# Optimization experiments

Hardware: AMD Instinct MI355X
Metric: run time of the kernel (lower is better)

## Reference

```python
import jax, jax.numpy as jnp
import numpy as np

THRESH = 1.0
SLOPE = 25.0  # fast_sigmoid surrogate slope
B, T, C_IN = 64, 512, 32
HID, TS, K = 128, 4, 3
C_OUT = HID * TS

@jax.custom_vjp
def spike_fn(x):
    # Heaviside forward, fast-sigmoid surrogate backward (matches snntorch surrogate.fast_sigmoid(slope=25))
    return (x > 0).astype(x.dtype)

def _spike_fwd(x):
    return spike_fn(x), x

def _spike_bwd(x, g):
    return (g / (SLOPE * jnp.abs(x) + 1.0) ** 2,)

spike_fn.defvjp(_spike_fwd, _spike_bwd)


def setup_inputs() -> dict:
    key = jax.random.key(0)
    ks = jax.random.split(key, 4)
    return {
        "x": jax.random.normal(ks[0], (B, T, C_IN), jnp.float32),
        "conv_w": jax.random.normal(ks[1], (C_OUT, C_IN, K), jnp.float32) / np.sqrt(C_IN * K).astype(np.float32),
        "conv_b": jax.random.normal(ks[2], (C_OUT,), jnp.float32) * 0.01,
        "bn_gamma": jnp.ones((C_OUT,), jnp.float32),
        "bn_beta": jnp.zeros((C_OUT,), jnp.float32),
        "bn_mean": jax.random.normal(ks[3], (C_OUT,), jnp.float32) * 0.1,
        "bn_var": jnp.ones((C_OUT,), jnp.float32),
        "lif_beta": jnp.full((HID,), 0.9, jnp.float32),
    }


def reference(x, conv_w, conv_b, bn_gamma, bn_beta, bn_mean, bn_var, lif_beta):
    # Conv1d(input -> hidden*Ts, k=3, pad=1): x (B,T,C) -> NCH layout
    h = jax.lax.conv_general_dilated(
        x.transpose(0, 2, 1), conv_w, (1,), [(K // 2, K // 2)],
        dimension_numbers=("NCH", "OIH", "NCH"))  # (B, C_OUT, T)
    h = h + conv_b[None, :, None]
    # BatchNorm1d in eval mode (running stats)
    scale = bn_gamma * jax.lax.rsqrt(bn_var + 1e-5)
    h = (h - bn_mean[None, :, None]) * scale[None, :, None] + bn_beta[None, :, None]
    # (B, C_OUT, T) -> (B, T, Ts, HID) -> (Ts*T, B, HID) time-major spike input
    h = h.transpose(0, 2, 1).reshape(B, T * TS, HID).transpose(1, 0, 2)

    beta = jnp.clip(lif_beta, 0.0, 1.0)

    def step(mem, h_t):
        # snntorch Leaky (reset_mechanism='subtract'): reset from previous mem, detached
        reset = jax.lax.stop_gradient((mem > THRESH).astype(mem.dtype))
        mem = beta * mem + h_t - reset * THRESH
        spk = spike_fn(mem - THRESH)
        return mem, (spk, mem)

    mem0 = jnp.zeros((B, HID), x.dtype)
    _, (spk_rec, mem_rec) = jax.lax.scan(step, mem0, h)
    return spk_rec, mem_rec  # each (Ts*T, B, HID)
```

## Files before the change

kernel.cpp:

```cpp
#include <hip/hip_runtime.h>

#define T_LEN 512
#define CIN   32
#define HIDN  128
#define TSUB  4
#define NB    64
#define TT    64
#define NT2   2048
#define COLS  8192

#define HT_IDX(s, col, t) ((((size_t)(s) * COLS + (size_t)(col)) * T_LEN) + (size_t)(t))

__global__ __launch_bounds__(256) void conv_bn_kernel(
    const float* __restrict__ x,
    const float* __restrict__ w,
    const float* __restrict__ cb,
    const float* __restrict__ gam,
    const float* __restrict__ bet,
    const float* __restrict__ mean,
    const float* __restrict__ var,
    float* __restrict__ hT)
{
    __shared__ float xs[66 * 36];
    __shared__ float ws[64 * 100];
    __shared__ float scs[64];
    __shared__ float bbs[64];

    const int t0  = blockIdx.x * TT;
    const int sg  = blockIdx.y;
    const int s   = sg >> 1;
    const int ch0 = (sg & 1) * 64;
    const int b   = blockIdx.z;
    const int tid = threadIdx.x;

    for (int idx = tid; idx < 66 * 32; idx += 256) {
        int r = idx >> 5, ci = idx & 31;
        int t = t0 + r - 1;
        xs[r * 36 + ci] = (t >= 0 && t < T_LEN) ? x[(b * T_LEN + t) * CIN + ci] : 0.0f;
    }
    for (int idx = tid; idx < 64 * 96; idx += 256) {
        int row = idx / 96, j = idx - row * 96;
        int k = j >> 5, i = j & 31;
        ws[row * 100 + j] = w[(s * HIDN + ch0 + row) * (CIN * 3) + i * 3 + k];
    }
    if (tid < 64) {
        int c = s * HIDN + ch0 + tid;
        float sc = gam[c] * rsqrtf(var[c] + 1e-5f);
        scs[tid] = sc;
        bbs[tid] = (cb[c] - mean[c]) * sc + bet[c];
    }
    __syncthreads();

    const int tc = tid & 31;
    const int tt = tid >> 5;

    float acc[2][8];
#pragma unroll
    for (int a = 0; a < 2; ++a)
#pragma unroll
        for (int q = 0; q < 8; ++q) acc[a][q] = 0.0f;

    for (int j0 = 0; j0 < 96; j0 += 4) {
        const int k  = j0 >> 5;
        const int i0 = j0 & 31;
        float4 wv[2];
#pragma unroll
        for (int cc = 0; cc < 2; ++cc)
            wv[cc] = *reinterpret_cast<const float4*>(&ws[(tc + cc * 32) * 100 + j0]);
#pragma unroll
        for (int tq = 0; tq < 8; ++tq) {
            float4 xv = *reinterpret_cast<const float4*>(&xs[(tt * 8 + tq + k) * 36 + i0]);
#pragma unroll
            for (int cc = 0; cc < 2; ++cc) {
                acc[cc][tq] = fmaf(wv[cc].x, xv.x, acc[cc][tq]);
                acc[cc][tq] = fmaf(wv[cc].y, xv.y, acc[cc][tq]);
                acc[cc][tq] = fmaf(wv[cc].z, xv.z, acc[cc][tq]);
                acc[cc][tq] = fmaf(wv[cc].w, xv.w, acc[cc][tq]);
            }
        }
    }

#pragma unroll
    for (int cc = 0; cc < 2; ++cc) {
        const int cl = tc + cc * 32;
        const float sc = scs[cl], bb = bbs[cl];
        float4 v0, v1;
        v0.x = fmaf(acc[cc][0], sc, bb);
        v0.y = fmaf(acc[cc][1], sc, bb);
        v0.z = fmaf(acc[cc][2], sc, bb);
        v0.w = fmaf(acc[cc][3], sc, bb);
        v1.x = fmaf(acc[cc][4], sc, bb);
        v1.y = fmaf(acc[cc][5], sc, bb);
        v1.z = fmaf(acc[cc][6], sc, bb);
        v1.w = fmaf(acc[cc][7], sc, bb);
        float* dst = hT + HT_IDX(s, b * HIDN + ch0 + cl, t0 + tt * 8);
        *reinterpret_cast<float4*>(dst)     = v0;
        *reinterpret_cast<float4*>(dst + 4) = v1;
    }
}

#define LIF_STEP(HVAL) { \
    const float reset = (mem > 1.0f) ? 1.0f : 0.0f; \
    mem = __fsub_rn(__fadd_rn(__fmul_rn(beta, mem), (HVAL)), reset); }

#define SLOT16(B) { \
    LIF_STEP((hq##B##0).x) LIF_STEP((hq##B##1).x) LIF_STEP((hq##B##2).x) LIF_STEP((hq##B##3).x) \
    LIF_STEP((hq##B##0).y) LIF_STEP((hq##B##1).y) LIF_STEP((hq##B##2).y) LIF_STEP((hq##B##3).y) \
    LIF_STEP((hq##B##0).z) LIF_STEP((hq##B##1).z) LIF_STEP((hq##B##2).z) LIF_STEP((hq##B##3).z) \
    LIF_STEP((hq##B##0).w) LIF_STEP((hq##B##1).w) LIF_STEP((hq##B##2).w) LIF_STEP((hq##B##3).w) \
    { const int tp = (m0 + B) * 16 + 15; \
      if (tp < NT2 - 1) memo[(size_t)tp * COLS + col] = mem; } \
    if (m0 + B + 4 < 128) { \
        hq##B##0 = p0[m0 + B + 4]; hq##B##1 = p1[m0 + B + 4]; \
        hq##B##2 = p2[m0 + B + 4]; hq##B##3 = p3[m0 + B + 4]; } }

__global__ __launch_bounds__(64) void lif_pass1_kernel(
    const float* __restrict__ hT,
    const float* __restrict__ lifb,
    float* __restrict__ out)
{
    const int col = blockIdx.x * 64 + threadIdx.x;
    const int hid = col & (HIDN - 1);
    float beta = fminf(fmaxf(lifb[hid], 0.0f), 1.0f);

    float* __restrict__ memo = out + (size_t)NT2 * COLS;

    const float4* p0 = reinterpret_cast<const float4*>(hT + HT_IDX(0, col, 0));
    const float4* p1 = reinterpret_cast<const float4*>(hT + HT_IDX(1, col, 0));
    const float4* p2 = reinterpret_cast<const float4*>(hT + HT_IDX(2, col, 0));
    const float4* p3 = reinterpret_cast<const float4*>(hT + HT_IDX(3, col, 0));

    float4 hq00 = p0[0], hq01 = p1[0], hq02 = p2[0], hq03 = p3[0];
    float4 hq10 = p0[1], hq11 = p1[1], hq12 = p2[1], hq13 = p3[1];
    float4 hq20 = p0[2], hq21 = p1[2], hq22 = p2[2], hq23 = p3[2];
    float4 hq30 = p0[3], hq31 = p1[3], hq32 = p2[3], hq33 = p3[3];

    float mem = 0.0f;

    for (int m0 = 0; m0 < 128; m0 += 4) {
        SLOT16(0)
        SLOT16(1)
        SLOT16(2)
        SLOT16(3)
    }
}

#define P2_STEP(HV0, HV1, J) { \
    const float r0 = (m0v > 1.0f) ? 1.0f : 0.0f; \
    const float r1 = (m1v > 1.0f) ? 1.0f : 0.0f; \
    m0v = __fsub_rn(__fadd_rn(__fmul_rn(b0, m0v), (HV0)), r0); \
    m1v = __fsub_rn(__fadd_rn(__fmul_rn(b1, m1v), (HV1)), r1); \
    const size_t o = (size_t)(tpb + (J)) * COLS + col0; \
    *reinterpret_cast<float2*>(spk + o)  = \
        make_float2((m0v > 1.0f) ? 1.0f : 0.0f, (m1v > 1.0f) ? 1.0f : 0.0f); \
    *reinterpret_cast<float2*>(memo + o) = make_float2(m0v, m1v); }

__global__ __launch_bounds__(256) void lif_pass2_kernel(
    const float* __restrict__ hT,
    const float* __restrict__ lifb,
    float* __restrict__ out)
{
    const int chunk = blockIdx.y;
    const int c2    = blockIdx.x * 256 + threadIdx.x;
    const int col0  = c2 * 2;
    const float b0 = fminf(fmaxf(lifb[col0 & (HIDN - 1)], 0.0f), 1.0f);
    const float b1 = fminf(fmaxf(lifb[(col0 + 1) & (HIDN - 1)], 0.0f), 1.0f);

    float* __restrict__ spk  = out;
    float* __restrict__ memo = out + (size_t)NT2 * COLS;

    const int tpb = chunk * 16;
    const int tb  = tpb >> 2;

    const float4 a0 = *reinterpret_cast<const float4*>(hT + HT_IDX(0, col0, tb));
    const float4 a1 = *reinterpret_cast<const float4*>(hT + HT_IDX(1, col0, tb));
    const float4 a2 = *reinterpret_cast<const float4*>(hT + HT_IDX(2, col0, tb));
    const float4 a3 = *reinterpret_cast<const float4*>(hT + HT_IDX(3, col0, tb));
    const float4 c0 = *reinterpret_cast<const float4*>(hT + HT_IDX(0, col0 + 1, tb));
    const float4 c1 = *reinterpret_cast<const float4*>(hT + HT_IDX(1, col0 + 1, tb));
    const float4 c2v= *reinterpret_cast<const float4*>(hT + HT_IDX(2, col0 + 1, tb));
    const float4 c3 = *reinterpret_cast<const float4*>(hT + HT_IDX(3, col0 + 1, tb));

    float m0v = 0.0f, m1v = 0.0f;
    if (chunk != 0) {
        const float2 ck = *reinterpret_cast<const float2*>(
            memo + (size_t)(tpb - 1) * COLS + col0);
        m0v = ck.x;
        m1v = ck.y;
    }

    P2_STEP(a0.x, c0.x,  0) P2_STEP(a1.x, c1.x,  1) P2_STEP(a2.x, c2v.x,  2) P2_STEP(a3.x, c3.x,  3)
    P2_STEP(a0.y, c0.y,  4) P2_STEP(a1.y, c1.y,  5) P2_STEP(a2.y, c2v.y,  6) P2_STEP(a3.y, c3.y,  7)
    P2_STEP(a0.z, c0.z,  8) P2_STEP(a1.z, c1.z,  9) P2_STEP(a2.z, c2v.z, 10) P2_STEP(a3.z, c3.z, 11)
    P2_STEP(a0.w, c0.w, 12) P2_STEP(a1.w, c1.w, 13) P2_STEP(a2.w, c2v.w, 14) P2_STEP(a3.w, c3.w, 15)
}

extern "C" void kernel_launch(void* const* d_in, const int* in_sizes, int n_in,
                              void* d_out, int out_size, void* d_ws, size_t ws_size,
                              hipStream_t stream) {
    const float* x    = (const float*)d_in[0];
    const float* w    = (const float*)d_in[1];
    const float* cb   = (const float*)d_in[2];
    const float* gam  = (const float*)d_in[3];
    const float* bet  = (const float*)d_in[4];
    const float* mean = (const float*)d_in[5];
    const float* var  = (const float*)d_in[6];
    const float* lifb = (const float*)d_in[7];

    float* hT = (float*)d_ws;

    dim3 gA(T_LEN / TT, 8, NB);
    conv_bn_kernel<<<gA, 256, 0, stream>>>(x, w, cb, gam, bet, mean, var, hT);

    lif_pass1_kernel<<<COLS / 64, 64, 0, stream>>>(hT, lifb, (float*)d_out);

    dim3 gC(COLS / 2 / 256, NT2 / 16);
    lif_pass2_kernel<<<gC, 256, 0, stream>>>(hT, lifb, (float*)d_out);
}
```

Baseline: 262.0 us.

## Widen LIF checkpoint chunks to 64 steps with triple-buffered scan prefetch

The sequential pass 1 now keeps three 64-step batches of inputs in flight in registers, which deepens the load prefetch and writes a membrane checkpoint every 64 steps instead of every 16. Pass 2 now has each thread replay a 64-step chunk for a single column instead of a 16-step chunk for two columns, so it launches fewer blocks and reads fewer checkpoints. Pass 2 stores become scalar per-column writes (coalesced across threads), and each thread does four times more serial work. Register pressure in pass 1 rises considerably.

```diff
diff --git a/kernel.cpp b/kernel.cpp
--- a/kernel.cpp
+++ b/kernel.cpp
@@ -8,6 +8,8 @@
 #define TT    64
 #define NT2   2048
 #define COLS  8192
+#define CHUNK 64
+#define NSS   32
 
 #define HT_IDX(s, col, t) ((((size_t)(s) * COLS + (size_t)(col)) * T_LEN) + (size_t)(t))
 
@@ -103,16 +105,25 @@
     const float reset = (mem > 1.0f) ? 1.0f : 0.0f; \
     mem = __fsub_rn(__fadd_rn(__fmul_rn(beta, mem), (HVAL)), reset); }
 
-#define SLOT16(B) { \
-    LIF_STEP((hq##B##0).x) LIF_STEP((hq##B##1).x) LIF_STEP((hq##B##2).x) LIF_STEP((hq##B##3).x) \
-    LIF_STEP((hq##B##0).y) LIF_STEP((hq##B##1).y) LIF_STEP((hq##B##2).y) LIF_STEP((hq##B##3).y) \
-    LIF_STEP((hq##B##0).z) LIF_STEP((hq##B##1).z) LIF_STEP((hq##B##2).z) LIF_STEP((hq##B##3).z) \
-    LIF_STEP((hq##B##0).w) LIF_STEP((hq##B##1).w) LIF_STEP((hq##B##2).w) LIF_STEP((hq##B##3).w) \
-    { const int tp = (m0 + B) * 16 + 15; \
-      if (tp < NT2 - 1) memo[(size_t)tp * COLS + col] = mem; } \
-    if (m0 + B + 4 < 128) { \
-        hq##B##0 = p0[m0 + B + 4]; hq##B##1 = p1[m0 + B + 4]; \
-        hq##B##2 = p2[m0 + B + 4]; hq##B##3 = p3[m0 + B + 4]; } }
+#define DECL_SS(P) float4 P##00,P##01,P##02,P##03, P##10,P##11,P##12,P##13, \
+                          P##20,P##21,P##22,P##23, P##30,P##31,P##32,P##33;
+
+#define LOAD_SS(P, SS) { \
+    P##00=p0[(SS)*4+0]; P##01=p0[(SS)*4+1]; P##02=p0[(SS)*4+2]; P##03=p0[(SS)*4+3]; \
+    P##10=p1[(SS)*4+0]; P##11=p1[(SS)*4+1]; P##12=p1[(SS)*4+2]; P##13=p1[(SS)*4+3]; \
+    P##20=p2[(SS)*4+0]; P##21=p2[(SS)*4+1]; P##22=p2[(SS)*4+2]; P##23=p2[(SS)*4+3]; \
+    P##30=p3[(SS)*4+0]; P##31=p3[(SS)*4+1]; P##32=p3[(SS)*4+2]; P##33=p3[(SS)*4+3]; }
+
+#define EATQUAD(P, Q) \
+    LIF_STEP((P##0##Q).x) LIF_STEP((P##1##Q).x) LIF_STEP((P##2##Q).x) LIF_STEP((P##3##Q).x) \
+    LIF_STEP((P##0##Q).y) LIF_STEP((P##1##Q).y) LIF_STEP((P##2##Q).y) LIF_STEP((P##3##Q).y) \
+    LIF_STEP((P##0##Q).z) LIF_STEP((P##1##Q).z) LIF_STEP((P##2##Q).z) LIF_STEP((P##3##Q).z) \
+    LIF_STEP((P##0##Q).w) LIF_STEP((P##1##Q).w) LIF_STEP((P##2##Q).w) LIF_STEP((P##3##Q).w)
+
+#define EAT_SS(P) EATQUAD(P,0) EATQUAD(P,1) EATQUAD(P,2) EATQUAD(P,3)
+
+#define CKPT(SSV) { const int tp = (SSV) * CHUNK + (CHUNK - 1); \
+    if (tp < NT2 - 1) memo[(size_t)tp * COLS + col] = mem; }
 
 __global__ __launch_bounds__(64) void lif_pass1_kernel(
     const float* __restrict__ hT,
@@ -130,30 +141,38 @@
     const float4* p2 = reinterpret_cast<const float4*>(hT + HT_IDX(2, col, 0));
     const float4* p3 = reinterpret_cast<const float4*>(hT + HT_IDX(3, col, 0));
 
-    float4 hq00 = p0[0], hq01 = p1[0], hq02 = p2[0], hq03 = p3[0];
-    float4 hq10 = p0[1], hq11 = p1[1], hq12 = p2[1], hq13 = p3[1];
-    float4 hq20 = p0[2], hq21 = p1[2], hq22 = p2[2], hq23 = p3[2];
-    float4 hq30 = p0[3], hq31 = p1[3], hq32 = p2[3], hq33 = p3[3];
+    DECL_SS(rA) DECL_SS(rB) DECL_SS(rC)
+
+    LOAD_SS(rA, 0)
+    LOAD_SS(rB, 1)
+    LOAD_SS(rC, 2)
 
     float mem = 0.0f;
 
-    for (int m0 = 0; m0 < 128; m0 += 4) {
-        SLOT16(0)
-        SLOT16(1)
-        SLOT16(2)
-        SLOT16(3)
-    }
-}
-
-#define P2_STEP(HV0, HV1, J) { \
-    const float r0 = (m0v > 1.0f) ? 1.0f : 0.0f; \
-    const float r1 = (m1v > 1.0f) ? 1.0f : 0.0f; \
-    m0v = __fsub_rn(__fadd_rn(__fmul_rn(b0, m0v), (HV0)), r0); \
-    m1v = __fsub_rn(__fadd_rn(__fmul_rn(b1, m1v), (HV1)), r1); \
-    const size_t o = (size_t)(tpb + (J)) * COLS + col0; \
-    *reinterpret_cast<float2*>(spk + o)  = \
-        make_float2((m0v > 1.0f) ? 1.0f : 0.0f, (m1v > 1.0f) ? 1.0f : 0.0f); \
-    *reinterpret_cast<float2*>(memo + o) = make_float2(m0v, m1v); }
+    for (int ss = 0; ss < NSS - 2; ss += 3) {
+        EAT_SS(rA) CKPT(ss)
+        if (ss + 3 < NSS) LOAD_SS(rA, ss + 3)
+        EAT_SS(rB) CKPT(ss + 1)
+        if (ss + 4 < NSS) LOAD_SS(rB, ss + 4)
+        EAT_SS(rC) CKPT(ss + 2)
+        if (ss + 5 < NSS) LOAD_SS(rC, ss + 5)
+    }
+    EAT_SS(rA) CKPT(30)
+    EAT_SS(rB)
+}
+
+#define P2_STEP(HV, J) { \
+    const float reset = (mem > 1.0f) ? 1.0f : 0.0f; \
+    mem = __fsub_rn(__fadd_rn(__fmul_rn(beta, mem), (HV)), reset); \
+    const size_t o = (size_t)(tpb + (J)) * COLS + col; \
+    spk[o]  = (mem > 1.0f) ? 1.0f : 0.0f; \
+    memo[o] = mem; }
+
+#define P2QUAD(Q) \
+    P2_STEP((q0##Q).x, (Q)*16+ 0) P2_STEP((q1##Q).x, (Q)*16+ 1) P2_STEP((q2##Q).x, (Q)*16+ 2) P2_STEP((q3##Q).x, (Q)*16+ 3) \
+    P2_STEP((q0##Q).y, (Q)*16+ 4) P2_STEP((q1##Q).y, (Q)*16+ 5) P2_STEP((q2##Q).y, (Q)*16+ 6) P2_STEP((q3##Q).y, (Q)*16+ 7) \
+    P2_STEP((q0##Q).z, (Q)*16+ 8) P2_STEP((q1##Q).z, (Q)*16+ 9) P2_STEP((q2##Q).z, (Q)*16+10) P2_STEP((q3##Q).z, (Q)*16+11) \
+    P2_STEP((q0##Q).w, (Q)*16+12) P2_STEP((q1##Q).w, (Q)*16+13) P2_STEP((q2##Q).w, (Q)*16+14) P2_STEP((q3##Q).w, (Q)*16+15)
 
 __global__ __launch_bounds__(256) void lif_pass2_kernel(
     const float* __restrict__ hT,
@@ -161,38 +180,28 @@
     float* __restrict__ out)
 {
     const int chunk = blockIdx.y;
-    const int c2    = blockIdx.x * 256 + threadIdx.x;
-    const int col0  = c2 * 2;
-    const float b0 = fminf(fmaxf(lifb[col0 & (HIDN - 1)], 0.0f), 1.0f);
-    const float b1 = fminf(fmaxf(lifb[(col0 + 1) & (HIDN - 1)], 0.0f), 1.0f);
+    const int col   = blockIdx.x * 256 + threadIdx.x;
+    const int hid   = col & (HIDN - 1);
+    float beta = fminf(fmaxf(lifb[hid], 0.0f), 1.0f);
 
     float* __restrict__ spk  = out;
     float* __restrict__ memo = out + (size_t)NT2 * COLS;
 
-    const int tpb = chunk * 16;
+    const int tpb = chunk * CHUNK;
     const int tb  = tpb >> 2;
 
-    const float4 a0 = *reinterpret_cast<const float4*>(hT + HT_IDX(0, col0, tb));
-    const float4 a1 = *reinterpret_cast<const float4*>(hT + HT_IDX(1, col0, tb));
-    const float4 a2 = *reinterpret_cast<const float4*>(hT + HT_IDX(2, col0, tb));
-    const float4 a3 = *reinterpret_cast<const float4*>(hT + HT_IDX(3, col0, tb));
-    const float4 c0 = *reinterpret_cast<const float4*>(hT + HT_IDX(0, col0 + 1, tb));
-    const float4 c1 = *reinterpret_cast<const float4*>(hT + HT_IDX(1, col0 + 1, tb));
-    const float4 c2v= *reinterpret_cast<const float4*>(hT + HT_IDX(2, col0 + 1, tb));
-    const float4 c3 = *reinterpret_cast<const float4*>(hT + HT_IDX(3, col0 + 1, tb));
-
-    float m0v = 0.0f, m1v = 0.0f;
-    if (chunk != 0) {
-        const float2 ck = *reinterpret_cast<const float2*>(
-            memo + (size_t)(tpb - 1) * COLS + col0);
-        m0v = ck.x;
-        m1v = ck.y;
-    }
-
-    P2_STEP(a0.x, c0.x,  0) P2_STEP(a1.x, c1.x,  1) P2_STEP(a2.x, c2v.x,  2) P2_STEP(a3.x, c3.x,  3)
-    P2_STEP(a0.y, c0.y,  4) P2_STEP(a1.y, c1.y,  5) P2_STEP(a2.y, c2v.y,  6) P2_STEP(a3.y, c3.y,  7)
-    P2_STEP(a0.z, c0.z,  8) P2_STEP(a1.z, c1.z,  9) P2_STEP(a2.z, c2v.z, 10) P2_STEP(a3.z, c3.z, 11)
-    P2_STEP(a0.w, c0.w, 12) P2_STEP(a1.w, c1.w, 13) P2_STEP(a2.w, c2v.w, 14) P2_STEP(a3.w, c3.w, 15)
+    const float4* b0 = reinterpret_cast<const float4*>(hT + HT_IDX(0, col, tb));
+    const float4* b1 = reinterpret_cast<const float4*>(hT + HT_IDX(1, col, tb));
+    const float4* b2 = reinterpret_cast<const float4*>(hT + HT_IDX(2, col, tb));
+    const float4* b3 = reinterpret_cast<const float4*>(hT + HT_IDX(3, col, tb));
+    const float4 q00 = b0[0], q01 = b0[1], q02 = b0[2], q03 = b0[3];
+    const float4 q10 = b1[0], q11 = b1[1], q12 = b1[2], q13 = b1[3];
+    const float4 q20 = b2[0], q21 = b2[1], q22 = b2[2], q23 = b2[3];
+    const float4 q30 = b3[0], q31 = b3[1], q32 = b3[2], q33 = b3[3];
+
+    float mem = (chunk == 0) ? 0.0f : memo[(size_t)(tpb - 1) * COLS + col];
+
+    P2QUAD(0) P2QUAD(1) P2QUAD(2) P2QUAD(3)
 }
 
 extern "C" void kernel_launch(void* const* d_in, const int* in_sizes, int n_in,
@@ -214,6 +223,6 @@
 
     lif_pass1_kernel<<<COLS / 64, 64, 0, stream>>>(hT, lifb, (float*)d_out);
 
-    dim3 gC(COLS / 2 / 256, NT2 / 16);
+    dim3 gC(COLS / 256, NT2 / CHUNK);
     lif_pass2_kernel<<<gC, 256, 0, stream>>>(hT, lifb, (float*)d_out);
 }
```

Result: faster. 256.0 us (-2.3%).
